# Kernel tuning notes

Measured on AMD Instinct MI355X. Metric: run time of the kernel, lower is better.

## Reference

```python
import jax, jax.numpy as jnp
import numpy as np
import math

B, S, D, H, FF = 8, 1024, 1024, 16, 4096
DH = D // H
EPS = 1e-5


def _layernorm(x, g, b):
    mu = jnp.mean(x, axis=-1, keepdims=True)
    var = jnp.mean((x - mu) ** 2, axis=-1, keepdims=True)
    return (x - mu) * jax.lax.rsqrt(var + EPS) * g + b


def _gelu_tanh(x):
    c = math.sqrt(2.0 / math.pi)
    return 0.5 * x * (1.0 + jnp.tanh(c * (x + 0.044715 * x ** 3)))


def setup_inputs() -> dict:
    key = jax.random.key(0)
    ks = jax.random.split(key, 8)
    s = lambda d: 1.0 / math.sqrt(d)
    return {
        "x": jax.random.normal(ks[0], (B, S, D), jnp.float32),
        "ln1_g": jnp.ones((D,), jnp.float32),
        "ln1_b": jnp.zeros((D,), jnp.float32),
        "w_qkv": jax.random.normal(ks[1], (3 * D, D), jnp.float32) * s(D),
        "b_qkv": jax.random.normal(ks[2], (3 * D,), jnp.float32) * 0.02,
        "w_o": jax.random.normal(ks[3], (D, D), jnp.float32) * s(D),
        "b_o": jax.random.normal(ks[4], (D,), jnp.float32) * 0.02,
        "ln2_g": jnp.ones((D,), jnp.float32),
        "ln2_b": jnp.zeros((D,), jnp.float32),
        "w1": jax.random.normal(ks[5], (FF, D), jnp.float32) * s(D),
        "b1": jax.random.normal(ks[6], (FF,), jnp.float32) * 0.02,
        "w2": jax.random.normal(ks[7], (D, FF), jnp.float32) * s(FF),
        "b2": jnp.zeros((D,), jnp.float32),
    }


def reference(x, ln1_g, ln1_b, w_qkv, b_qkv, w_o, b_o, ln2_g, ln2_b, w1, b1, w2, b2):
    # --- pre-LN causal self-attention ---
    h = _layernorm(x, ln1_g, ln1_b)
    qkv = h @ w_qkv.T + b_qkv                      # [B,S,3D]
    q, k, v = jnp.split(qkv, 3, axis=-1)
    q = q.reshape(B, S, H, DH)
    k = k.reshape(B, S, H, DH)
    v = v.reshape(B, S, H, DH)
    scores = jnp.einsum("bqhd,bkhd->bhqk", q, k) / math.sqrt(DH)
    causal = jnp.triu(jnp.ones((S, S), jnp.bool_), 1)  # True above diagonal
    scores = jnp.where(causal, -jnp.inf, scores)
    attn = jax.nn.softmax(scores, axis=-1)
    o = jnp.einsum("bhqk,bkhd->bqhd", attn, v).reshape(B, S, D)
    x = x + (o @ w_o.T + b_o)
    # --- FFN ---
    h = _layernorm(x, ln2_g, ln2_b)
    h = _gelu_tanh(h @ w1.T + b1) @ w2.T + b2
    return x + h
```

## Files before the change

### kernel.cpp

```cpp
#include <hip/hip_runtime.h>
#include <math.h>


typedef __bf16 bf16_t;
typedef __bf16 bf16x4 __attribute__((ext_vector_type(4)));
typedef __bf16 bf16x8 __attribute__((ext_vector_type(8)));
typedef float f32x4 __attribute__((ext_vector_type(4)));

#define WAITVM(N) asm volatile("s_waitcnt vmcnt(" #N ")" ::: "memory")
#define WAITLGKM0 asm volatile("s_waitcnt lgkmcnt(0)" ::: "memory")
#define SCHEDBAR __builtin_amdgcn_sched_barrier(0)

__device__ __forceinline__ void async16(const void* g, void* l) {
    __builtin_amdgcn_global_load_lds(
        (const __attribute__((address_space(1))) void*)g,
        (__attribute__((address_space(3))) void*)l,
        16, 0, 0);
}

__device__ __forceinline__ void ln_row(const float* __restrict__ x,
                                       const float* __restrict__ g,
                                       const float* __restrict__ bb,
                                       bf16_t* __restrict__ out, int row) {
    const int tid = threadIdx.x;
    const float4 xv = *(const float4*)(x + row * 1024 + tid * 4);
    float s1 = xv.x + xv.y + xv.z + xv.w;
    float s2 = xv.x * xv.x + xv.y * xv.y + xv.z * xv.z + xv.w * xv.w;
#pragma unroll
    for (int m = 32; m >= 1; m >>= 1) {
        s1 += __shfl_xor(s1, m);
        s2 += __shfl_xor(s2, m);
    }
    __shared__ float r1[4], r2[4];
    const int wid = tid >> 6, lane = tid & 63;
    if (lane == 0) { r1[wid] = s1; r2[wid] = s2; }
    __syncthreads();
    s1 = r1[0] + r1[1] + r1[2] + r1[3];
    s2 = r2[0] + r2[1] + r2[2] + r2[3];
    const float mu = s1 * (1.0f / 1024.0f);
    const float var = s2 * (1.0f / 1024.0f) - mu * mu;
    const float rs = rsqrtf(var + 1e-5f);
    const float4 gv = *(const float4*)(g + tid * 4);
    const float4 bv = *(const float4*)(bb + tid * 4);
    bf16x4 o;
    o[0] = (bf16_t)((xv.x - mu) * rs * gv.x + bv.x);
    o[1] = (bf16_t)((xv.y - mu) * rs * gv.y + bv.y);
    o[2] = (bf16_t)((xv.z - mu) * rs * gv.z + bv.z);
    o[3] = (bf16_t)((xv.w - mu) * rs * gv.w + bv.w);
    *(bf16x4*)(out + row * 1024 + tid * 4) = o;
}

__global__ __launch_bounds__(256) void prep(
    const float* __restrict__ s0, const float* __restrict__ s1,
    const float* __restrict__ s2, const float* __restrict__ s3,
    bf16_t* __restrict__ d0, bf16_t* __restrict__ d1,
    bf16_t* __restrict__ d2, bf16_t* __restrict__ d3,
    const float* __restrict__ x, const float* __restrict__ ln1g,
    const float* __restrict__ ln1b, bf16_t* __restrict__ h) {
    if (blockIdx.x >= 12288) {
        ln_row(x, ln1g, ln1b, h, blockIdx.x - 12288);
        return;
    }
    const int g = blockIdx.x * 256 + threadIdx.x;
    const float* s;
    bf16_t* d;
    int off;
    if (g < 786432)       { s = s0; d = d0; off = g; }
    else if (g < 1048576) { s = s1; d = d1; off = g - 786432; }
    else if (g < 2097152) { s = s2; d = d2; off = g - 1048576; }
    else                  { s = s3; d = d3; off = g - 2097152; }
    const int i = off * 4;
    const float4 v = *(const float4*)(s + i);
    bf16x4 o;
    o[0] = (bf16_t)v.x; o[1] = (bf16_t)v.y; o[2] = (bf16_t)v.z; o[3] = (bf16_t)v.w;
    *(bf16x4*)(d + i) = o;
}

__global__ __launch_bounds__(256) void ln_b(const bf16_t* __restrict__ x,
                                            const float* __restrict__ g,
                                            const float* __restrict__ bb,
                                            bf16_t* __restrict__ out) {
    const int tid = threadIdx.x;
    const int row = blockIdx.x;
    const bf16x4 xb = *(const bf16x4*)(x + row * 1024 + tid * 4);
    const float x0 = (float)xb[0], x1 = (float)xb[1], x2 = (float)xb[2], x3 = (float)xb[3];
    float s1 = x0 + x1 + x2 + x3;
    float s2 = x0 * x0 + x1 * x1 + x2 * x2 + x3 * x3;
#pragma unroll
    for (int m = 32; m >= 1; m >>= 1) {
        s1 += __shfl_xor(s1, m);
        s2 += __shfl_xor(s2, m);
    }
    __shared__ float r1[4], r2[4];
    const int wid = tid >> 6, lane = tid & 63;
    if (lane == 0) { r1[wid] = s1; r2[wid] = s2; }
    __syncthreads();
    s1 = r1[0] + r1[1] + r1[2] + r1[3];
    s2 = r2[0] + r2[1] + r2[2] + r2[3];
    const float mu = s1 * (1.0f / 1024.0f);
    const float var = s2 * (1.0f / 1024.0f) - mu * mu;
    const float rs = rsqrtf(var + 1e-5f);
    const float4 gv = *(const float4*)(g + tid * 4);
    const float4 bv = *(const float4*)(bb + tid * 4);
    bf16x4 o;
    o[0] = (bf16_t)((x0 - mu) * rs * gv.x + bv.x);
    o[1] = (bf16_t)((x1 - mu) * rs * gv.y + bv.y);
    o[2] = (bf16_t)((x2 - mu) * rs * gv.z + bv.z);
    o[3] = (bf16_t)((x3 - mu) * rs * gv.w + bv.w);
    *(bf16x4*)(out + row * 1024 + tid * 4) = o;
}

template <int MODE>
__global__ __launch_bounds__(256, 2) void gemm_bt(
    const bf16_t* __restrict__ A, const bf16_t* __restrict__ W,
    const float* __restrict__ bias, const float* __restrict__ residf,
    const bf16_t* __restrict__ residb,
    bf16_t* __restrict__ outb, float* __restrict__ outf,
    bf16_t* __restrict__ vt, int N, int K) {
    __shared__ bf16_t As[128 * 64];
    __shared__ bf16_t Bs[128 * 64];
    const int tid = threadIdx.x;
    const int w = tid >> 6;
    const int lane = tid & 63;
    const int l15 = lane & 15;
    const int quad = lane >> 4;

    const int nbn = N >> 7;
    const int per = 8 * nbn;
    const int lid = blockIdx.x;
    const int bm = (lid / per) * 8 + (lid % per) % 8;
    const int bn = (lid % per) / 8;
    const int m0 = bm * 128;
    const int n0 = bn * 128;
    const int wm = (w & 1) * 64;
    const int wn = (w >> 1) * 64;

    int rr[4], so[4];
#pragma unroll
    for (int q = 0; q < 4; q++) {
        const int c = q * 256 + w * 64 + lane;
        rr[q] = c >> 3;
        so[q] = ((c & 7) ^ (rr[q] & 7)) * 8;
    }
    const bf16_t* pA[4];
    const bf16_t* pB[4];
#pragma unroll
    for (int q = 0; q < 4; q++) {
        pA[q] = A + (size_t)(m0 + rr[q]) * K + so[q];
        pB[q] = W + (size_t)(n0 + rr[q]) * K + so[q];
    }

    f32x4 acc[4][4] = {};

    for (int k0 = 0; k0 < K; k0 += 64) {
#pragma unroll
        for (int q = 0; q < 4; q++) {
            async16(pA[q], As + q * 2048 + w * 512);
            async16(pB[q], Bs + q * 2048 + w * 512);
            pA[q] += 64; pB[q] += 64;
        }
        __syncthreads();

        bf16x8 af[4][2], bfr[4][2];
#pragma unroll
        for (int i = 0; i < 4; i++) {
            const int r = wm + i * 16 + l15;
#pragma unroll
            for (int f = 0; f < 2; f++) {
                const int slot = (f * 4 + quad) ^ (r & 7);
                af[i][f] = *(const bf16x8*)(As + r * 64 + slot * 8);
            }
        }
#pragma unroll
        for (int j = 0; j < 4; j++) {
            const int r = wn + j * 16 + l15;
#pragma unroll
            for (int f = 0; f < 2; f++) {
                const int slot = (f * 4 + quad) ^ (r & 7);
                bfr[j][f] = *(const bf16x8*)(Bs + r * 64 + slot * 8);
            }
        }
#pragma unroll
        for (int i = 0; i < 4; i++)
#pragma unroll
            for (int j = 0; j < 4; j++)
#pragma unroll
                for (int f = 0; f < 2; f++)
                    acc[i][j] = __builtin_amdgcn_mfma_f32_16x16x32_bf16(
                        af[i][f], bfr[j][f], acc[i][j], 0, 0, 0);
        __syncthreads();
    }

#pragma unroll
    for (int i = 0; i < 4; i++) {
#pragma unroll
        for (int j = 0; j < 4; j++) {
            const int col = n0 + wn + j * 16 + l15;
            const float bcol = bias[col];
            const int row0 = m0 + wm + i * 16 + quad * 4;
            float v4[4];
#pragma unroll
            for (int q = 0; q < 4; q++) {
                float v = acc[i][j][q] + bcol;
                if (MODE == 1) {
                    const float u2 = -1.5957691216057308f * (v + 0.044715f * v * v * v);
                    v = v * __builtin_amdgcn_rcpf(1.0f + __expf(u2));
                }
                v4[q] = v;
            }
            if (MODE == 4) {
#pragma unroll
                for (int q = 0; q < 4; q++) {
                    const size_t idx = (size_t)(row0 + q) * N + col;
                    outb[idx] = (bf16_t)(v4[q] + residf[idx]);
                }
            } else if (MODE == 5) {
#pragma unroll
                for (int q = 0; q < 4; q++) {
                    const size_t idx = (size_t)(row0 + q) * N + col;
                    outf[idx] = v4[q] + (float)residb[idx];
                }
            } else if (MODE == 3 && col >= 2048) {
                const int bh = (row0 >> 10) * 16 + ((col - 2048) >> 6);
                const int d = (col - 2048) & 63;
                bf16x4 pk;
#pragma unroll
                for (int q = 0; q < 4; q++) pk[q] = (bf16_t)v4[q];
                *(bf16x4*)(vt + (size_t)bh * 65536 + d * 1024 + (row0 & 1023)) = pk;
            } else {
#pragma unroll
                for (int q = 0; q < 4; q++)
                    outb[(size_t)(row0 + q) * N + col] = (bf16_t)v4[q];
            }
        }
    }
}

template <int MODE>
__global__ __launch_bounds__(512, 2) void gemm8(
    const bf16_t* __restrict__ A, const bf16_t* __restrict__ W,
    const float* __restrict__ bias, bf16_t* __restrict__ outb,
    bf16_t* __restrict__ vt, int N, int K) {
    __shared__ bf16_t lds[65536];
    const int tid = threadIdx.x;
    const int w = tid >> 6, lane = tid & 63;
    const int l15 = lane & 15, quad = lane >> 4;
    const int wr = w >> 2, wc = w & 3;

    const int nwg = gridDim.x;
    const int wg = (blockIdx.x & 7) * (nwg >> 3) + (blockIdx.x >> 3);
    const int nbn = N >> 8;
    const int per = 8 * nbn;
    const int bm = (wg / per) * 8 + (wg % per) % 8;
    const int bn = (wg % per) / 8;
    const int m0 = bm << 8, n0 = bn << 8;

    int r_[2], s_[2];
#pragma unroll
    for (int L = 0; L < 2; L++) {
        const int c = L * 512 + tid;
        r_[L] = c >> 3;
        s_[L] = ((c & 7) ^ (r_[L] & 7)) * 8;
    }
    const bf16_t* pa0[2]; const bf16_t* pa1[2];
    const bf16_t* pb0[2]; const bf16_t* pb1[2];
#pragma unroll
    for (int L = 0; L < 2; L++) {
        pa0[L] = A + (size_t)(m0 + r_[L]) * K + s_[L];
        pa1[L] = pa0[L] + (size_t)128 * K;
        pb0[L] = W + (size_t)(n0 + r_[L]) * K + s_[L];
        pb1[L] = pb0[L] + (size_t)128 * K;
    }

    const int fragoff = wr * 4096 + l15 * 64;
    const int swz0 = (quad ^ (l15 & 7)) * 8;
    const int swz1 = ((4 + quad) ^ (l15 & 7)) * 8;
    const bf16_t* bA0 = lds + fragoff + swz0;
    const bf16_t* bA1 = lds + fragoff + swz1;
    const bf16_t* bB0 = lds + 16384 + wc * 2048 + l15 * 64 + swz0;
    const bf16_t* bB1 = lds + 16384 + wc * 2048 + l15 * 64 + swz1;
    const bf16_t* cA0 = bA0 + 32768;
    const bf16_t* cA1 = bA1 + 32768;
    const bf16_t* cB0 = bB0 + 32768;
    const bf16_t* cB1 = bB1 + 32768;

    f32x4 acc[8][4] = {};
    bf16x8 af[4][2], bfr[4][2];

    async16(pa0[0], lds + w * 512);
    async16(pa0[1], lds + 4096 + w * 512);
    async16(pb0[0], lds + 16384 + w * 512);
    async16(pb0[1], lds + 20480 + w * 512);
    async16(pb1[0], lds + 24576 + w * 512);
    async16(pb1[1], lds + 28672 + w * 512);
    async16(pa1[0], lds + 8192 + w * 512);
    async16(pa1[1], lds + 12288 + w * 512);
    WAITVM(4);
    __builtin_amdgcn_s_barrier();

    const int NT = K >> 6;
    for (int t = 0; t < NT - 1; ++t) {
        bf16_t* nb = (bf16_t*)(cA0 - (fragoff + swz0));
        const int kn = (t + 1) << 6;

#pragma unroll
        for (int i = 0; i < 4; i++) {
            af[i][0] = *(const bf16x8*)(bA0 + i * 1024);
            af[i][1] = *(const bf16x8*)(bA1 + i * 1024);
        }
#pragma unroll
        for (int j = 0; j < 2; j++) {
            bfr[j][0] = *(const bf16x8*)(bB0 + j * 1024);
            bfr[j][1] = *(const bf16x8*)(bB1 + j * 1024);
        }
        async16(pa0[0] + kn, nb + w * 512);
        async16(pa0[1] + kn, nb + 4096 + w * 512);
        SCHEDBAR;
        __builtin_amdgcn_s_barrier();
        WAITLGKM0;
        SCHEDBAR;
        __builtin_amdgcn_s_setprio(1);
#pragma unroll
        for (int i = 0; i < 4; i++)
#pragma unroll
            for (int j = 0; j < 2; j++)
#pragma unroll
                for (int f = 0; f < 2; f++)
                    acc[i][j] = __builtin_amdgcn_mfma_f32_16x16x32_bf16(af[i][f], bfr[j][f], acc[i][j], 0, 0, 0);
        __builtin_amdgcn_s_setprio(0);
        SCHEDBAR;
        WAITVM(4);
        __builtin_amdgcn_s_barrier();

#pragma unroll
        for (int j = 2; j < 4; j++) {
            bfr[j][0] = *(const bf16x8*)(bB0 + 8192 + (j & 1) * 1024);
            bfr[j][1] = *(const bf16x8*)(bB1 + 8192 + (j & 1) * 1024);
        }
        async16(pb0[0] + kn, nb + 16384 + w * 512);
        async16(pb0[1] + kn, nb + 20480 + w * 512);
        SCHEDBAR;
        __builtin_amdgcn_s_barrier();
        WAITLGKM0;
        SCHEDBAR;
        __builtin_amdgcn_s_setprio(1);
#pragma unroll
        for (int i = 0; i < 4; i++)
#pragma unroll
            for (int j = 2; j < 4; j++)
#pragma unroll
                for (int f = 0; f < 2; f++)
                    acc[i][j] = __builtin_amdgcn_mfma_f32_16x16x32_bf16(af[i][f], bfr[j][f], acc[i][j], 0, 0, 0);
        __builtin_amdgcn_s_setprio(0);
        SCHEDBAR;
        WAITVM(4);
        __builtin_amdgcn_s_barrier();

#pragma unroll
        for (int i = 0; i < 4; i++) {
            af[i][0] = *(const bf16x8*)(bA0 + 8192 + i * 1024);
            af[i][1] = *(const bf16x8*)(bA1 + 8192 + i * 1024);
        }
        async16(pb1[0] + kn, nb + 24576 + w * 512);
        async16(pb1[1] + kn, nb + 28672 + w * 512);
        SCHEDBAR;
        __builtin_amdgcn_s_barrier();
        WAITLGKM0;
        SCHEDBAR;
        __builtin_amdgcn_s_setprio(1);
#pragma unroll
        for (int i = 0; i < 4; i++)
#pragma unroll
            for (int j = 0; j < 2; j++)
#pragma unroll
                for (int f = 0; f < 2; f++)
                    acc[i + 4][j] = __builtin_amdgcn_mfma_f32_16x16x32_bf16(af[i][f], bfr[j][f], acc[i + 4][j], 0, 0, 0);
        __builtin_amdgcn_s_setprio(0);
        SCHEDBAR;
        __builtin_amdgcn_s_barrier();

        async16(pa1[0] + kn, nb + 8192 + w * 512);
        async16(pa1[1] + kn, nb + 12288 + w * 512);
        SCHEDBAR;
        __builtin_amdgcn_s_setprio(1);
#pragma unroll
        for (int i = 0; i < 4; i++)
#pragma unroll
            for (int j = 2; j < 4; j++)
#pragma unroll
                for (int f = 0; f < 2; f++)
                    acc[i + 4][j] = __builtin_amdgcn_mfma_f32_16x16x32_bf16(af[i][f], bfr[j][f], acc[i + 4][j], 0, 0, 0);
        __builtin_amdgcn_s_setprio(0);
        SCHEDBAR;
        WAITVM(4);
        __builtin_amdgcn_s_barrier();

        { const bf16_t* s;
          s = bA0; bA0 = cA0; cA0 = s;
          s = bA1; bA1 = cA1; cA1 = s;
          s = bB0; bB0 = cB0; cB0 = s;
          s = bB1; bB1 = cB1; cB1 = s; }
    }

    {
#pragma unroll
        for (int i = 0; i < 4; i++) {
            af[i][0] = *(const bf16x8*)(bA0 + i * 1024);
            af[i][1] = *(const bf16x8*)(bA1 + i * 1024);
        }
#pragma unroll
        for (int j = 0; j < 2; j++) {
            bfr[j][0] = *(const bf16x8*)(bB0 + j * 1024);
            bfr[j][1] = *(const bf16x8*)(bB1 + j * 1024);
        }
        SCHEDBAR;
        __builtin_amdgcn_s_barrier();
        WAITLGKM0;
        SCHEDBAR;
        __builtin_amdgcn_s_setprio(1);
#pragma unroll
        for (int i = 0; i < 4; i++)
#pragma unroll
            for (int j = 0; j < 2; j++)
#pragma unroll
                for (int f = 0; f < 2; f++)
                    acc[i][j] = __builtin_amdgcn_mfma_f32_16x16x32_bf16(af[i][f], bfr[j][f], acc[i][j], 0, 0, 0);
        __builtin_amdgcn_s_setprio(0);
        SCHEDBAR;
        WAITVM(2);
        __builtin_amdgcn_s_barrier();
#pragma unroll
        for (int j = 2; j < 4; j++) {
            bfr[j][0] = *(const bf16x8*)(bB0 + 8192 + (j & 1) * 1024);
            bfr[j][1] = *(const bf16x8*)(bB1 + 8192 + (j & 1) * 1024);
        }
        SCHEDBAR;
        __builtin_amdgcn_s_barrier();
        WAITLGKM0;
        SCHEDBAR;
        __builtin_amdgcn_s_setprio(1);
#pragma unroll
        for (int i = 0; i < 4; i++)
#pragma unroll
            for (int j = 2; j < 4; j++)
#pragma unroll
                for (int f = 0; f < 2; f++)
                    acc[i][j] = __builtin_amdgcn_mfma_f32_16x16x32_bf16(af[i][f], bfr[j][f], acc[i][j], 0, 0, 0);
        __builtin_amdgcn_s_setprio(0);
        SCHEDBAR;
        WAITVM(0);
        __builtin_amdgcn_s_barrier();
#pragma unroll
        for (int i = 0; i < 4; i++) {
            af[i][0] = *(const bf16x8*)(bA0 + 8192 + i * 1024);
            af[i][1] = *(const bf16x8*)(bA1 + 8192 + i * 1024);
        }
        WAITLGKM0;
        SCHEDBAR;
        __builtin_amdgcn_s_setprio(1);
#pragma unroll
        for (int i = 0; i < 4; i++)
#pragma unroll
            for (int j = 0; j < 4; j++)
#pragma unroll
                for (int f = 0; f < 2; f++)
                    acc[i + 4][j] = __builtin_amdgcn_mfma_f32_16x16x32_bf16(af[i][f], bfr[j][f], acc[i + 4][j], 0, 0, 0);
        __builtin_amdgcn_s_setprio(0);
    }

#pragma unroll
    for (int i = 0; i < 8; i++) {
        const int row0 = m0 + (i >> 2) * 128 + wr * 64 + (i & 3) * 16 + quad * 4;
#pragma unroll
        for (int j = 0; j < 4; j++) {
            const int col = n0 + (j >> 1) * 128 + wc * 32 + (j & 1) * 16 + l15;
            const float bcol = bias[col];
            float v4[4];
#pragma unroll
            for (int q = 0; q < 4; q++) {
                float v = acc[i][j][q] + bcol;
                if (MODE == 1) {
                    const float u2 = -1.5957691216057308f * (v + 0.044715f * v * v * v);
                    v = v * __builtin_amdgcn_rcpf(1.0f + __expf(u2));
                }
                v4[q] = v;
            }
            if (MODE == 3 && col >= 2048) {
                const int bh = (row0 >> 10) * 16 + ((col - 2048) >> 6);
                const int d = (col - 2048) & 63;
                bf16x4 pk;
#pragma unroll
                for (int q = 0; q < 4; q++) pk[q] = (bf16_t)v4[q];
                *(bf16x4*)(vt + (size_t)bh * 65536 + d * 1024 + (row0 & 1023)) = pk;
            } else {
#pragma unroll
                for (int q = 0; q < 4; q++)
                    outb[(size_t)(row0 + q) * N + col] = (bf16_t)v4[q];
            }
        }
    }
}

__global__ __launch_bounds__(512) void attn_mfma(const bf16_t* __restrict__ qkv,
                                                 const bf16_t* __restrict__ vt,
                                                 bf16_t* __restrict__ o) {
    __shared__ bf16_t Ks[4096];
    __shared__ bf16_t Vs[4096];
    __shared__ bf16_t Ps[8][32][72];
    const int tid = threadIdx.x;
    const int w = tid >> 6;
    const int lane = tid & 63;
    const int l15 = lane & 15;
    const int quad = lane >> 4;
    const int qb = blockIdx.x;
    const int bh = blockIdx.y;
    const int b = bh >> 4, h = bh & 15;

    const int qrow = b * 1024 + qb * 256 + w * 32;

    bf16x8 qf[2][2];
#pragma unroll
    for (int g = 0; g < 2; g++)
#pragma unroll
        for (int f = 0; f < 2; f++) {
            bf16x8 t = *(const bf16x8*)(qkv + (size_t)(qrow + g * 16 + l15) * 3072 + h * 64 + f * 32 + quad * 8);
#pragma unroll
            for (int e = 0; e < 8; e++) t[e] = (bf16_t)((float)t[e] * 0.125f);
            qf[g][f] = t;
        }

    f32x4 Ot[2][4] = {};
    float mrow[2] = {-3.0e38f, -3.0e38f};
    float lrow[2] = {0.0f, 0.0f};

    const int c0 = w * 64 + lane;
    const int r0 = c0 >> 3, g0 = (((c0 & 7) ^ (r0 & 7))) * 8;

    const bf16_t* kbase = qkv + (size_t)(b * 1024) * 3072 + 1024 + h * 64;
    const bf16_t* vbase = vt + (size_t)bh * 64 * 1024;

    const int ktmax = 4 * qb + 3;
    for (int kt = 0; kt <= ktmax; kt++) {
        async16(kbase + (size_t)(kt * 64 + r0) * 3072 + g0, Ks + w * 512);
        async16(vbase + (size_t)r0 * 1024 + kt * 64 + g0, Vs + w * 512);
        __syncthreads();

#pragma unroll
        for (int g = 0; g < 2; g++) {
            const int qmaxw = qb * 256 + w * 32 + g * 16 + 15;
            if (kt * 64 > qmaxw) continue;
            const int ktd = qmaxw >> 6;
            const int kbd = (2 * w + g) & 3;

            f32x4 sf[4];
#pragma unroll
            for (int kb = 0; kb < 4; kb++) {
                if (kt * 64 + kb * 16 > qmaxw) {
                    sf[kb] = (f32x4){-3.0e38f, -3.0e38f, -3.0e38f, -3.0e38f};
                    continue;
                }
                const int r = kb * 16 + l15;
                f32x4 acc = {};
#pragma unroll
                for (int f = 0; f < 2; f++) {
                    const int seg = (f * 4 + quad) ^ (r & 7);
                    const bf16x8 kf = *(const bf16x8*)(Ks + r * 64 + seg * 8);
                    acc = __builtin_amdgcn_mfma_f32_16x16x32_bf16(kf, qf[g][f], acc, 0, 0, 0);
                }
                if (kt == ktd && kb == kbd) {
#pragma unroll
                    for (int rr2 = 0; rr2 < 4; rr2++)
                        if (quad * 4 + rr2 > l15) acc[rr2] = -3.0e38f;
                }
                sf[kb] = acc;
            }

            float tmax = -3.0e38f;
#pragma unroll
            for (int kb = 0; kb < 4; kb++)
#pragma unroll
                for (int rr2 = 0; rr2 < 4; rr2++) tmax = fmaxf(tmax, sf[kb][rr2]);
            tmax = fmaxf(tmax, __shfl_xor(tmax, 16));
            tmax = fmaxf(tmax, __shfl_xor(tmax, 32));
            const float mnew = fmaxf(mrow[g], tmax);
            const float alpha = __expf(mrow[g] - mnew);
            float psum = 0.0f;
#pragma unroll
            for (int kb = 0; kb < 4; kb++) {
                bf16x4 pk;
#pragma unroll
                for (int rr2 = 0; rr2 < 4; rr2++) {
                    const float p = __expf(sf[kb][rr2] - mnew);
                    psum += p;
                    pk[rr2] = (bf16_t)p;
                }
                *(bf16x4*)(&Ps[w][g * 16 + l15][kb * 16 + quad * 4]) = pk;
            }
            psum += __shfl_xor(psum, 16);
            psum += __shfl_xor(psum, 32);
            lrow[g] = lrow[g] * alpha + psum;
            mrow[g] = mnew;
#pragma unroll
            for (int db = 0; db < 4; db++)
#pragma unroll
                for (int rr2 = 0; rr2 < 4; rr2++) Ot[g][db][rr2] *= alpha;

#pragma unroll
            for (int ks = 0; ks < 2; ks++) {
                if (kt * 64 + ks * 32 > qmaxw) break;
                const bf16x8 pf = *(const bf16x8*)(&Ps[w][g * 16 + l15][ks * 32 + quad * 8]);
#pragma unroll
                for (int db = 0; db < 4; db++) {
                    const int d = db * 16 + l15;
                    const int seg = (ks * 4 + quad) ^ (d & 7);
                    const bf16x8 vf = *(const bf16x8*)(Vs + d * 64 + seg * 8);
                    Ot[g][db] = __builtin_amdgcn_mfma_f32_16x16x32_bf16(vf, pf, Ot[g][db], 0, 0, 0);
                }
            }
        }
        __syncthreads();
    }

#pragma unroll
    for (int g = 0; g < 2; g++) {
        const float rl = 1.0f / lrow[g];
#pragma unroll
        for (int db = 0; db < 4; db++) {
            bf16x4 ov;
#pragma unroll
            for (int rr2 = 0; rr2 < 4; rr2++) ov[rr2] = (bf16_t)(Ot[g][db][rr2] * rl);
            *(bf16x4*)(o + (size_t)(qrow + g * 16 + l15) * 1024 + h * 64 + db * 16 + quad * 4) = ov;
        }
    }
}

extern "C" void kernel_launch(void* const* d_in, const int* in_sizes, int n_in,
                              void* d_out, int out_size, void* d_ws, size_t ws_size,
                              hipStream_t stream) {
    const float* x     = (const float*)d_in[0];
    const float* ln1g  = (const float*)d_in[1];
    const float* ln1b  = (const float*)d_in[2];
    const float* w_qkv = (const float*)d_in[3];
    const float* b_qkv = (const float*)d_in[4];
    const float* w_o   = (const float*)d_in[5];
    const float* b_o   = (const float*)d_in[6];
    const float* ln2g  = (const float*)d_in[7];
    const float* ln2b  = (const float*)d_in[8];
    const float* w1    = (const float*)d_in[9];
    const float* b1    = (const float*)d_in[10];
    const float* w2    = (const float*)d_in[11];
    const float* b2    = (const float*)d_in[12];
    float* out = (float*)d_out;

    char* w = (char*)d_ws;
    bf16_t* wbqkv = (bf16_t*)(w + 0);
    bf16_t* wbo   = (bf16_t*)(w + 6291456);
    bf16_t* wb1   = (bf16_t*)(w + 8388608);
    bf16_t* wb2   = (bf16_t*)(w + 16777216);
    bf16_t* h     = (bf16_t*)(w + 25165824);
    bf16_t* qkv   = (bf16_t*)(w + 41943040);
    bf16_t* ob    = (bf16_t*)(w + 92274688);
    bf16_t* x1b   = (bf16_t*)(w + 109051904);
    bf16_t* f     = (bf16_t*)(w + 142606336);
    bf16_t* vtb   = (bf16_t*)(w + 142606336);

    prep<<<20480, 256, 0, stream>>>(w_qkv, w_o, w1, w2, wbqkv, wbo, wb1, wb2,
                                    x, ln1g, ln1b, h);
    gemm8<3><<<384, 512, 0, stream>>>(h, wbqkv, b_qkv, qkv, vtb, 3072, 1024);
    attn_mfma<<<dim3(4, 128), 512, 0, stream>>>(qkv, vtb, ob);
    gemm_bt<4><<<64 * 8, 256, 0, stream>>>(ob, wbo, b_o, x, nullptr, x1b, nullptr, nullptr, 1024, 1024);
    ln_b<<<8192, 256, 0, stream>>>(x1b, ln2g, ln2b, h);
    gemm8<1><<<512, 512, 0, stream>>>(h, wb1, b1, f, nullptr, 4096, 1024);
    gemm_bt<5><<<64 * 8, 256, 0, stream>>>(f, wb2, b2, nullptr, x1b, nullptr, out, nullptr, 1024, 4096);
}
```

Before: 436.2 us.

## Replace gemm_bt with double-buffered 128x256 pipelined GEMM for out-proj and FFN2

Swaps the single-buffered 128x128 GEMM used for the output projection and the second FFN matmul for a 512-thread kernel with 128x256 tiles. It double-buffers LDS and issues the next K-tile's async global-to-LDS loads between two MFMA phases. It also adds explicit waitcnt/barrier scheduling, setprio around MFMA bursts, and an XCD-aware block remap. The aim is to hide global load latency and cut barrier stalls, at the cost of half as many workgroups (256) and more LDS per block, which may reduce occupancy.

```diff
diff --git a/kernel.cpp b/kernel.cpp
--- a/kernel.cpp
+++ b/kernel.cpp
@@ -111,126 +111,193 @@
 }
 
 template <int MODE>
-__global__ __launch_bounds__(256, 2) void gemm_bt(
+__global__ __launch_bounds__(512, 2) void gemm2p(
     const bf16_t* __restrict__ A, const bf16_t* __restrict__ W,
     const float* __restrict__ bias, const float* __restrict__ residf,
     const bf16_t* __restrict__ residb,
-    bf16_t* __restrict__ outb, float* __restrict__ outf,
-    bf16_t* __restrict__ vt, int N, int K) {
-    __shared__ bf16_t As[128 * 64];
-    __shared__ bf16_t Bs[128 * 64];
+    bf16_t* __restrict__ outb, float* __restrict__ outf, int N, int K) {
+    __shared__ bf16_t lds[49152];
     const int tid = threadIdx.x;
-    const int w = tid >> 6;
-    const int lane = tid & 63;
-    const int l15 = lane & 15;
-    const int quad = lane >> 4;
-
-    const int nbn = N >> 7;
+    const int w = tid >> 6, lane = tid & 63;
+    const int l15 = lane & 15, quad = lane >> 4;
+    const int wm = (w & 1) * 64;
+    const int wc = w >> 1;
+
+    const int nwg = gridDim.x;
+    const int wg = (blockIdx.x & 7) * (nwg >> 3) + (blockIdx.x >> 3);
+    const int nbn = N >> 8;
     const int per = 8 * nbn;
-    const int lid = blockIdx.x;
-    const int bm = (lid / per) * 8 + (lid % per) % 8;
-    const int bn = (lid % per) / 8;
-    const int m0 = bm * 128;
-    const int n0 = bn * 128;
-    const int wm = (w & 1) * 64;
-    const int wn = (w >> 1) * 64;
-
-    int rr[4], so[4];
-#pragma unroll
-    for (int q = 0; q < 4; q++) {
-        const int c = q * 256 + w * 64 + lane;
-        rr[q] = c >> 3;
-        so[q] = ((c & 7) ^ (rr[q] & 7)) * 8;
-    }
-    const bf16_t* pA[4];
-    const bf16_t* pB[4];
-#pragma unroll
-    for (int q = 0; q < 4; q++) {
-        pA[q] = A + (size_t)(m0 + rr[q]) * K + so[q];
-        pB[q] = W + (size_t)(n0 + rr[q]) * K + so[q];
-    }
+    const int bm = (wg / per) * 8 + (wg % per) % 8;
+    const int bn = (wg % per) / 8;
+    const int m0 = bm << 7, n0 = bn << 8;
+
+    const bf16_t* pa[2]; const bf16_t* pb[4];
+#pragma unroll
+    for (int L = 0; L < 2; L++) {
+        const int c = L * 512 + tid, r = c >> 3;
+        pa[L] = A + (size_t)(m0 + r) * K + ((c & 7) ^ (r & 7)) * 8;
+    }
+#pragma unroll
+    for (int L = 0; L < 4; L++) {
+        const int c = L * 512 + tid, r = c >> 3;
+        pb[L] = W + (size_t)(n0 + r) * K + ((c & 7) ^ (r & 7)) * 8;
+    }
+
+    const int swz0 = (quad ^ (l15 & 7)) * 8;
+    const int swz1 = ((4 + quad) ^ (l15 & 7)) * 8;
+    const int fragoffA = wm * 64 + l15 * 64 + swz0;
+    const bf16_t* bA0 = lds + fragoffA;
+    const bf16_t* bA1 = lds + wm * 64 + l15 * 64 + swz1;
+    const bf16_t* bB0 = lds + 8192 + wc * 2048 + l15 * 64 + swz0;
+    const bf16_t* bB1 = lds + 8192 + wc * 2048 + l15 * 64 + swz1;
+    const bf16_t* cA0 = bA0 + 24576;
+    const bf16_t* cA1 = bA1 + 24576;
+    const bf16_t* cB0 = bB0 + 24576;
+    const bf16_t* cB1 = bB1 + 24576;
 
     f32x4 acc[4][4] = {};
-
-    for (int k0 = 0; k0 < K; k0 += 64) {
-#pragma unroll
-        for (int q = 0; q < 4; q++) {
-            async16(pA[q], As + q * 2048 + w * 512);
-            async16(pB[q], Bs + q * 2048 + w * 512);
-            pA[q] += 64; pB[q] += 64;
-        }
-        __syncthreads();
-
-        bf16x8 af[4][2], bfr[4][2];
+    bf16x8 af[4][2], bfr[4][2];
+
+    async16(pa[0], lds + w * 512);
+    async16(pa[1], lds + 4096 + w * 512);
+    async16(pb[0], lds + 8192 + w * 512);
+    async16(pb[1], lds + 12288 + w * 512);
+    async16(pb[2], lds + 16384 + w * 512);
+    async16(pb[3], lds + 20480 + w * 512);
+    WAITVM(2);
+    __builtin_amdgcn_s_barrier();
+
+    const int NT = K >> 6;
+    for (int t = 0; t < NT - 1; ++t) {
+        bf16_t* nb = (bf16_t*)(cA0 - fragoffA);
+        const int kn = (t + 1) << 6;
+
 #pragma unroll
         for (int i = 0; i < 4; i++) {
-            const int r = wm + i * 16 + l15;
-#pragma unroll
-            for (int f = 0; f < 2; f++) {
-                const int slot = (f * 4 + quad) ^ (r & 7);
-                af[i][f] = *(const bf16x8*)(As + r * 64 + slot * 8);
-            }
-        }
+            af[i][0] = *(const bf16x8*)(bA0 + i * 1024);
+            af[i][1] = *(const bf16x8*)(bA1 + i * 1024);
+        }
+#pragma unroll
+        for (int j = 0; j < 2; j++) {
+            bfr[j][0] = *(const bf16x8*)(bB0 + j * 1024);
+            bfr[j][1] = *(const bf16x8*)(bB1 + j * 1024);
+        }
+        async16(pa[0] + kn, nb + w * 512);
+        async16(pa[1] + kn, nb + 4096 + w * 512);
+        async16(pb[0] + kn, nb + 8192 + w * 512);
+        async16(pb[1] + kn, nb + 12288 + w * 512);
+        SCHEDBAR;
+        __builtin_amdgcn_s_barrier();
+        WAITLGKM0;
+        SCHEDBAR;
+        __builtin_amdgcn_s_setprio(1);
+#pragma unroll
+        for (int i = 0; i < 4; i++)
+#pragma unroll
+            for (int j = 0; j < 2; j++)
+#pragma unroll
+                for (int f = 0; f < 2; f++)
+                    acc[i][j] = __builtin_amdgcn_mfma_f32_16x16x32_bf16(af[i][f], bfr[j][f], acc[i][j], 0, 0, 0);
+        __builtin_amdgcn_s_setprio(0);
+        SCHEDBAR;
+        WAITVM(4);
+        __builtin_amdgcn_s_barrier();
+
+#pragma unroll
+        for (int j = 2; j < 4; j++) {
+            bfr[j][0] = *(const bf16x8*)(bB0 + 8192 + (j & 1) * 1024);
+            bfr[j][1] = *(const bf16x8*)(bB1 + 8192 + (j & 1) * 1024);
+        }
+        async16(pb[2] + kn, nb + 16384 + w * 512);
+        async16(pb[3] + kn, nb + 20480 + w * 512);
+        SCHEDBAR;
+        __builtin_amdgcn_s_barrier();
+        WAITLGKM0;
+        SCHEDBAR;
+        __builtin_amdgcn_s_setprio(1);
+#pragma unroll
+        for (int i = 0; i < 4; i++)
+#pragma unroll
+            for (int j = 2; j < 4; j++)
+#pragma unroll
+                for (int f = 0; f < 2; f++)
+                    acc[i][j] = __builtin_amdgcn_mfma_f32_16x16x32_bf16(af[i][f], bfr[j][f], acc[i][j], 0, 0, 0);
+        __builtin_amdgcn_s_setprio(0);
+        SCHEDBAR;
+        WAITVM(2);
+        __builtin_amdgcn_s_barrier();
+
+        { const bf16_t* s;
+          s = bA0; bA0 = cA0; cA0 = s;
+          s = bA1; bA1 = cA1; cA1 = s;
+          s = bB0; bB0 = cB0; cB0 = s;
+          s = bB1; bB1 = cB1; cB1 = s; }
+    }
+
+    {
+#pragma unroll
+        for (int i = 0; i < 4; i++) {
+            af[i][0] = *(const bf16x8*)(bA0 + i * 1024);
+            af[i][1] = *(const bf16x8*)(bA1 + i * 1024);
+        }
+#pragma unroll
+        for (int j = 0; j < 2; j++) {
+            bfr[j][0] = *(const bf16x8*)(bB0 + j * 1024);
+            bfr[j][1] = *(const bf16x8*)(bB1 + j * 1024);
+        }
+        SCHEDBAR;
+        __builtin_amdgcn_s_barrier();
+        WAITLGKM0;
+        SCHEDBAR;
+        __builtin_amdgcn_s_setprio(1);
+#pragma unroll
+        for (int i = 0; i < 4; i++)
+#pragma unroll
+            for (int j = 0; j < 2; j++)
+#pragma unroll
+                for (int f = 0; f < 2; f++)
+                    acc[i][j] = __builtin_amdgcn_mfma_f32_16x16x32_bf16(af[i][f], bfr[j][f], acc[i][j], 0, 0, 0);
+        __builtin_amdgcn_s_setprio(0);
+        SCHEDBAR;
+        WAITVM(0);
+        __builtin_amdgcn_s_barrier();
+#pragma unroll
+        for (int j = 2; j < 4; j++) {
+            bfr[j][0] = *(const bf16x8*)(bB0 + 8192 + (j & 1) * 1024);
+            bfr[j][1] = *(const bf16x8*)(bB1 + 8192 + (j & 1) * 1024);
+        }
+        WAITLGKM0;
+        SCHEDBAR;
+        __builtin_amdgcn_s_setprio(1);
+#pragma unroll
+        for (int i = 0; i < 4; i++)
+#pragma unroll
+            for (int j = 2; j < 4; j++)
+#pragma unroll
+                for (int f = 0; f < 2; f++)
+                    acc[i][j] = __builtin_amdgcn_mfma_f32_16x16x32_bf16(af[i][f], bfr[j][f], acc[i][j], 0, 0, 0);
+        __builtin_amdgcn_s_setprio(0);
+    }
+
+#pragma unroll
+    for (int i = 0; i < 4; i++) {
+        const int row0 = m0 + wm + i * 16 + quad * 4;
 #pragma unroll
         for (int j = 0; j < 4; j++) {
-            const int r = wn + j * 16 + l15;
-#pragma unroll
-            for (int f = 0; f < 2; f++) {
-                const int slot = (f * 4 + quad) ^ (r & 7);
-                bfr[j][f] = *(const bf16x8*)(Bs + r * 64 + slot * 8);
-            }
-        }
-#pragma unroll
-        for (int i = 0; i < 4; i++)
-#pragma unroll
-            for (int j = 0; j < 4; j++)
-#pragma unroll
-                for (int f = 0; f < 2; f++)
-                    acc[i][j] = __builtin_amdgcn_mfma_f32_16x16x32_bf16(
-                        af[i][f], bfr[j][f], acc[i][j], 0, 0, 0);
-        __syncthreads();
-    }
-
-#pragma unroll
-    for (int i = 0; i < 4; i++) {
-#pragma unroll
-        for (int j = 0; j < 4; j++) {
-            const int col = n0 + wn + j * 16 + l15;
+            const int col = n0 + (j >> 1) * 128 + wc * 32 + (j & 1) * 16 + l15;
             const float bcol = bias[col];
-            const int row0 = m0 + wm + i * 16 + quad * 4;
-            float v4[4];
-#pragma unroll
-            for (int q = 0; q < 4; q++) {
-                float v = acc[i][j][q] + bcol;
-                if (MODE == 1) {
-                    const float u2 = -1.5957691216057308f * (v + 0.044715f * v * v * v);
-                    v = v * __builtin_amdgcn_rcpf(1.0f + __expf(u2));
-                }
-                v4[q] = v;
-            }
             if (MODE == 4) {
 #pragma unroll
                 for (int q = 0; q < 4; q++) {
                     const size_t idx = (size_t)(row0 + q) * N + col;
-                    outb[idx] = (bf16_t)(v4[q] + residf[idx]);
+                    outb[idx] = (bf16_t)(acc[i][j][q] + bcol + residf[idx]);
                 }
-            } else if (MODE == 5) {
+            } else {
 #pragma unroll
                 for (int q = 0; q < 4; q++) {
                     const size_t idx = (size_t)(row0 + q) * N + col;
-                    outf[idx] = v4[q] + (float)residb[idx];
+                    outf[idx] = acc[i][j][q] + bcol + (float)residb[idx];
                 }
-            } else if (MODE == 3 && col >= 2048) {
-                const int bh = (row0 >> 10) * 16 + ((col - 2048) >> 6);
-                const int d = (col - 2048) & 63;
-                bf16x4 pk;
-#pragma unroll
-                for (int q = 0; q < 4; q++) pk[q] = (bf16_t)v4[q];
-                *(bf16x4*)(vt + (size_t)bh * 65536 + d * 1024 + (row0 & 1023)) = pk;
-            } else {
-#pragma unroll
-                for (int q = 0; q < 4; q++)
-                    outb[(size_t)(row0 + q) * N + col] = (bf16_t)v4[q];
             }
         }
     }
@@ -668,8 +735,8 @@
                                     x, ln1g, ln1b, h);
     gemm8<3><<<384, 512, 0, stream>>>(h, wbqkv, b_qkv, qkv, vtb, 3072, 1024);
     attn_mfma<<<dim3(4, 128), 512, 0, stream>>>(qkv, vtb, ob);
-    gemm_bt<4><<<64 * 8, 256, 0, stream>>>(ob, wbo, b_o, x, nullptr, x1b, nullptr, nullptr, 1024, 1024);
+    gemm2p<4><<<256, 512, 0, stream>>>(ob, wbo, b_o, x, nullptr, x1b, nullptr, 1024, 1024);
     ln_b<<<8192, 256, 0, stream>>>(x1b, ln2g, ln2b, h);
     gemm8<1><<<512, 512, 0, stream>>>(h, wb1, b1, f, nullptr, 4096, 1024);
-    gemm_bt<5><<<64 * 8, 256, 0, stream>>>(f, wb2, b2, nullptr, x1b, nullptr, out, nullptr, 1024, 4096);
+    gemm2p<5><<<256, 512, 0, stream>>>(f, wb2, b2, nullptr, x1b, nullptr, out, 1024, 4096);
 }
```

Measured after the change: 436.8 us. No clear change (+0.1%).
